# Kernel tuning notes

Measured on AMD Instinct MI355X. Metric: run time of the kernel, lower is better.

## Reference

```python
import jax, jax.numpy as jnp
import numpy as np

N = 50000      # nodes
E = 800000     # edges (avg degree 16)
D_IN = 18      # 3 fields x 6 timesteps
H = 128        # hidden_dim
HEADS = 4
DH = H // HEADS
D_OUT = 3
NEG = 0.2      # LeakyReLU slope
BN_EPS = 1e-5


def leaky(x):
    return jnp.where(x >= 0, x, NEG * x)


def segment_softmax(e, row, n):
    # numerically stable softmax over edges grouped by target node (axis 0)
    m = jax.ops.segment_max(e, row, num_segments=n)
    ex = jnp.exp(e - m[row])
    s = jax.ops.segment_sum(ex, row, num_segments=n)
    return ex / (s[row] + 1e-16)


def single_head_attn(x, row, col, Wv, b, a_src, a_dst):
    h = x @ Wv + b                                   # [N,H] values
    s_src = x @ a_src                                # [N] query scalar (dim=1)
    s_dst = x @ a_dst                                # [N] key scalar
    e = leaky(s_src[row] + s_dst[col])               # [E]
    alpha = segment_softmax(e, row, N)               # [E]
    return jax.ops.segment_sum(alpha[:, None] * h[col], row, num_segments=N)


def multi_head_attn(x, row, col, Wv, b, a_src, a_dst):
    h = jnp.einsum('nd,hde->nhe', x, Wv) + b         # [N,4,32] per-head values
    s_src = x @ a_src.T                              # [N,4] per-head Q (dim=1)
    s_dst = x @ a_dst.T                              # [N,4] per-head K (dim=1)
    e = leaky(s_src[row] + s_dst[col])               # [E,4]
    alpha = segment_softmax(e, row, N)               # [E,4]
    out = jax.ops.segment_sum(alpha[:, :, None] * h[col], row, num_segments=N)
    return out.reshape(N, HEADS * DH)                # concat heads -> [N,128]


def batch_norm_eval(x, g, bt, m, v):
    return (x - m) * jax.lax.rsqrt(v + BN_EPS) * g + bt


def setup_inputs() -> dict:
    key = jax.random.key(0)
    ks = jax.random.split(key, 16)
    rn = lambda k, shp, s=0.05: jax.random.normal(k, shp, dtype=jnp.float32) * s
    return {
        'x': rn(ks[0], (N, D_IN), 1.0),
        'edge_index': jax.random.randint(ks[1], (2, E), 0, N, dtype=jnp.int32),
        'W_in': rn(ks[2], (D_IN, H)),
        'b_in': jnp.zeros((H,), jnp.float32),
        'W_agg': rn(ks[3], (D_IN, H)),
        'b_agg': jnp.zeros((H,), jnp.float32),
        'sh_Wv': rn(ks[4], (2, H, H)),
        'sh_b': jnp.zeros((2, H), jnp.float32),
        'sh_asrc': rn(ks[5], (2, H)),
        'sh_adst': rn(ks[6], (2, H)),
        'mh_Wv': rn(ks[7], (HEADS, H, DH)),
        'mh_b': jnp.zeros((HEADS, DH), jnp.float32),
        'mh_asrc': rn(ks[8], (HEADS, H)),
        'mh_adst': rn(ks[9], (HEADS, H)),
        'bn_gamma': jnp.ones((3, H), jnp.float32),
        'bn_beta': jnp.zeros((3, H), jnp.float32),
        'bn_mean': jnp.zeros((3, H), jnp.float32),
        'bn_var': jnp.ones((3, H), jnp.float32),
        'W_o1': rn(ks[10], (H, H)),
        'b_o1': jnp.zeros((H,), jnp.float32),
        'W_o2': rn(ks[11], (H, D_OUT), 0.01),
        'b_o2': jnp.zeros((D_OUT,), jnp.float32),
    }


def reference(x, edge_index, W_in, b_in, W_agg, b_agg, sh_Wv, sh_b, sh_asrc, sh_adst,
              mh_Wv, mh_b, mh_asrc, mh_adst, bn_gamma, bn_beta, bn_mean, bn_var,
              W_o1, b_o1, W_o2, b_o2):
    row, col = edge_index[0], edge_index[1]

    # explicit neighbor mean aggregation (fused gather-scatter)
    nsum = jax.ops.segment_sum(x[col], row, num_segments=N)     # [N,D_IN]
    deg = jax.ops.segment_sum(jnp.ones((E,), x.dtype), row, num_segments=N)
    nmean = nsum / (deg[:, None] + 1e-8)

    h = (x @ W_in + b_in) + (nmean @ W_agg + b_agg)             # [N,H]
    x0 = h

    # layer 0: single-head attention + BN + residual(x0) + leaky
    h1 = single_head_attn(h, row, col, sh_Wv[0], sh_b[0], sh_asrc[0], sh_adst[0])
    h1 = batch_norm_eval(h1, bn_gamma[0], bn_beta[0], bn_mean[0], bn_var[0])
    h = leaky(x0 + h1)

    # layer 1: multi-head (4 heads, Q/K dim=1) + BN, no residual (i=1), leaky
    h2 = multi_head_attn(h, row, col, mh_Wv, mh_b, mh_asrc, mh_adst)
    h2 = batch_norm_eval(h2, bn_gamma[1], bn_beta[1], bn_mean[1], bn_var[1])
    h = leaky(h2)

    # layer 2: single-head + BN + residual + leaky
    r = h
    h3 = single_head_attn(h, row, col, sh_Wv[1], sh_b[1], sh_asrc[1], sh_adst[1])
    h3 = batch_norm_eval(h3, bn_gamma[2], bn_beta[2], bn_mean[2], bn_var[2])
    h = leaky(r + h3)

    # output head (dropout is a no-op in eval)
    delta = leaky(h @ W_o1 + b_o1) @ W_o2 + b_o2                # [N,3]

    # residual skip from last timestep of the input sequence
    return x[:, -D_OUT:] + delta
```

## Files before the change

### kernel.cpp

```cpp
#include <hip/hip_runtime.h>
#include <math.h>

#define DIN 18
#define HID 128
#define NEGS 0.2f
#define BN_EPS 1e-5f
#define SCHUNK 2048

typedef unsigned short ushort_t;
typedef __attribute__((ext_vector_type(8))) short bf16x8;
typedef __attribute__((ext_vector_type(4))) float f32x4;

__device__ __forceinline__ float leaky(float x){ return x >= 0.f ? x : NEGS * x; }

__device__ __forceinline__ float wred_sum(float v){
  #pragma unroll
  for (int off = 32; off; off >>= 1) v += __shfl_xor(v, off);
  return v;
}

__device__ __forceinline__ ushort_t f2bf(float f){
  union { float f; unsigned u; } v; v.f = f;
  unsigned r = v.u + 0x7FFFu + ((v.u >> 16) & 1u);
  return (ushort_t)(r >> 16);
}
__device__ __forceinline__ float bf_lo(unsigned p){ return __uint_as_float(p << 16); }
__device__ __forceinline__ float bf_hi(unsigned p){ return __uint_as_float(p & 0xFFFF0000u); }

__device__ __forceinline__ float sel4(float v0, float v1, float v2, float v3, int hd){
  float a = (hd & 1) ? v1 : v0;
  float b = (hd & 1) ? v3 : v2;
  return (hd & 2) ? b : a;
}

__global__ void k_deg(const int* __restrict__ row, int* __restrict__ deg, int E){
  int i = blockIdx.x * blockDim.x + threadIdx.x;
  if (i < E) atomicAdd(&deg[row[i]], 1);
}

__global__ void k_scan1(const int* __restrict__ deg, int* __restrict__ bsum, int n){
  __shared__ int wtot[4];
  int tid = threadIdx.x, lane = tid & 63, wid = tid >> 6;
  int base = blockIdx.x * SCHUNK + tid * 8;
  int acc = 0;
  #pragma unroll
  for (int j = 0; j < 8; ++j){
    int i = base + j;
    if (i < n) acc += deg[i];
  }
  #pragma unroll
  for (int off = 32; off; off >>= 1) acc += __shfl_xor(acc, off);
  if (lane == 0) wtot[wid] = acc;
  __syncthreads();
  if (tid == 0) bsum[blockIdx.x] = wtot[0] + wtot[1] + wtot[2] + wtot[3];
}

__global__ void k_scan2(int* __restrict__ bsum, int nb){
  int lane = threadIdx.x;
  int carry = 0;
  for (int base = 0; base < nb; base += 64){
    int i = base + lane;
    int v = (i < nb) ? bsum[i] : 0;
    #pragma unroll
    for (int off = 1; off < 64; off <<= 1){
      int u = __shfl_up(v, off);
      if (lane >= off) v += u;
    }
    if (i < nb) bsum[i] = v + carry;
    carry += __shfl(v, 63);
  }
}

__global__ void k_scan3(const int* __restrict__ deg, const int* __restrict__ bsum,
                        int* __restrict__ rowptr, int n){
  __shared__ int wtot[4];
  int tid = threadIdx.x, lane = tid & 63, wid = tid >> 6;
  int base = blockIdx.x * SCHUNK + tid * 8;
  int l[8];
  int acc = 0;
  #pragma unroll
  for (int j = 0; j < 8; ++j){
    int i = base + j;
    acc += (i < n) ? deg[i] : 0;
    l[j] = acc;
  }
  int v = acc;
  #pragma unroll
  for (int off = 1; off < 64; off <<= 1){
    int u = __shfl_up(v, off);
    if (lane >= off) v += u;
  }
  if (lane == 63) wtot[wid] = v;
  __syncthreads();
  int woff = 0;
  for (int w = 0; w < wid; ++w) woff += wtot[w];
  int boff = (blockIdx.x == 0) ? 0 : bsum[blockIdx.x - 1];
  int tpre = boff + woff + (v - acc);
  #pragma unroll
  for (int j = 0; j < 8; ++j){
    int i = base + j;
    if (i < n) rowptr[i + 1] = tpre + l[j];
  }
  if (blockIdx.x == 0 && tid == 0) rowptr[0] = 0;
}

__global__ void k_fill(const int* __restrict__ row, const int* __restrict__ col,
                       const int* __restrict__ rowptr, int* __restrict__ cursor,
                       int* __restrict__ cols_s, int E){
  int i = blockIdx.x * blockDim.x + threadIdx.x;
  if (i < E){
    int r = row[i];
    int p = atomicAdd(&cursor[r], 1);
    cols_s[rowptr[r] + p] = col[i];
  }
}

__global__ void k_nmean(const float* __restrict__ x, const int* __restrict__ rowptr,
                        const int* __restrict__ cols, float* __restrict__ nmean, int n){
  __shared__ int s_cv[4][64];
  int wid = threadIdx.x >> 6;
  int node = blockIdx.x * 4 + wid;
  if (node >= n) return;
  int lane = threadIdx.x & 63;
  int s = rowptr[node], e = rowptr[node + 1];
  float acc = 0.f;
  for (int j0 = s; j0 < e; j0 += 64){
    int len = min(64, e - j0);
    int cv = (lane < len) ? cols[j0 + lane] : 0;
    s_cv[wid][lane] = cv;
    int k = 0;
    for (; k + 4 <= len; k += 4){
      int c0 = s_cv[wid][k], c1 = s_cv[wid][k+1], c2 = s_cv[wid][k+2], c3 = s_cv[wid][k+3];
      if (lane < DIN){
        float v0 = x[c0 * DIN + lane], v1 = x[c1 * DIN + lane];
        float v2 = x[c2 * DIN + lane], v3 = x[c3 * DIN + lane];
        acc += (v0 + v1) + (v2 + v3);
      }
    }
    for (; k < len; ++k){
      int c = s_cv[wid][k];
      if (lane < DIN) acc += x[c * DIN + lane];
    }
  }
  if (lane < DIN){
    float d = (float)(e - s);
    nmean[node * DIN + lane] = acc / (d + 1e-8f);
  }
}

__global__ void k_h_in(const float* __restrict__ x, const float* __restrict__ nmean,
                       const float* __restrict__ Win, const float* __restrict__ bin,
                       const float* __restrict__ Wagg, const float* __restrict__ bagg,
                       float* __restrict__ out, int n){
  int wid = threadIdx.x >> 6;
  int node = blockIdx.x * 4 + wid;
  if (node >= n) return;
  int lane = threadIdx.x & 63;
  float xv = 0.f;
  if (lane < DIN) xv = x[node * DIN + lane];
  else if (lane < 2 * DIN) xv = nmean[node * DIN + (lane - DIN)];
  float acc0 = bin[lane]      + bagg[lane];
  float acc1 = bin[64 + lane] + bagg[64 + lane];
  #pragma unroll
  for (int d = 0; d < DIN; ++d){
    float xd = __shfl(xv, d);
    float nd = __shfl(xv, DIN + d);
    acc0 += xd * Win[d * HID + lane]       + nd * Wagg[d * HID + lane];
    acc1 += xd * Win[d * HID + 64 + lane]  + nd * Wagg[d * HID + 64 + lane];
  }
  out[node * HID + lane]      = acc0;
  out[node * HID + 64 + lane] = acc1;
}

__global__ void k_wt_sh(const float* __restrict__ W, ushort_t* __restrict__ Wt){
  int i = blockIdx.x * 256 + threadIdx.x;
  int c = i >> 7, d = i & 127;
  Wt[c * HID + d] = f2bf(W[d * HID + c]);
}
__global__ void k_wt_mh(const float* __restrict__ mhWv, ushort_t* __restrict__ Wt){
  int i = blockIdx.x * 256 + threadIdx.x;
  int c = i >> 7, d = i & 127;
  Wt[c * HID + d] = f2bf(mhWv[((c >> 5) * HID + d) * 32 + (c & 31)]);
}

__global__ void k_gemm_mfma(const float* __restrict__ A, const ushort_t* __restrict__ Bt,
                            const float* __restrict__ bias, ushort_t* __restrict__ dstb,
                            float* __restrict__ dstf, int n, int mode){
  int wv = threadIdx.x >> 6, lane = threadIdx.x & 63;
  int r0 = blockIdx.x * 64 + wv * 16;
  int lr = lane & 15, lk = lane >> 4;
  int arow = r0 + lr; if (arow >= n) arow = n - 1;
  const float* Ap = A + (size_t)arow * HID + lk * 8;
  bf16x8 a[4];
  #pragma unroll
  for (int kb = 0; kb < 4; ++kb){
    float4 lo = *(const float4*)(Ap + kb * 32);
    float4 hi = *(const float4*)(Ap + kb * 32 + 4);
    bf16x8 t;
    t[0] = (short)f2bf(lo.x); t[1] = (short)f2bf(lo.y);
    t[2] = (short)f2bf(lo.z); t[3] = (short)f2bf(lo.w);
    t[4] = (short)f2bf(hi.x); t[5] = (short)f2bf(hi.y);
    t[6] = (short)f2bf(hi.z); t[7] = (short)f2bf(hi.w);
    a[kb] = t;
  }
  f32x4 acc[8];
  #pragma unroll
  for (int t = 0; t < 8; ++t) acc[t] = (f32x4){0.f, 0.f, 0.f, 0.f};
  #pragma unroll
  for (int t = 0; t < 8; ++t){
    const ushort_t* Bp = Bt + (size_t)(t * 16 + lr) * HID + lk * 8;
    #pragma unroll
    for (int kb = 0; kb < 4; ++kb){
      bf16x8 b = *(const bf16x8*)(Bp + kb * 32);
      acc[t] = __builtin_amdgcn_mfma_f32_16x16x32_bf16(a[kb], b, acc[t], 0, 0, 0);
    }
  }
  #pragma unroll
  for (int t = 0; t < 8; ++t){
    int col = t * 16 + lr;
    float bs = bias[col];
    #pragma unroll
    for (int j = 0; j < 4; ++j){
      int rr = r0 + lk * 4 + j;
      if (rr < n){
        float v = acc[t][j] + bs;
        if (mode == 2) dstb[(size_t)rr * HID + col] = f2bf(v);
        else           dstf[(size_t)rr * HID + col] = leaky(v);
      }
    }
  }
}

__global__ void k_scores_sh(const float* __restrict__ h, const float* __restrict__ asrc,
                            const float* __restrict__ adst,
                            float* __restrict__ ssrc, float* __restrict__ sdst, int n){
  int node = blockIdx.x * 4 + (threadIdx.x >> 6);
  if (node >= n) return;
  int lane = threadIdx.x & 63;
  float h0 = h[node * HID + lane], h1 = h[node * HID + 64 + lane];
  float ps = h0 * asrc[lane] + h1 * asrc[64 + lane];
  float pd = h0 * adst[lane] + h1 * adst[64 + lane];
  ps = wred_sum(ps);
  pd = wred_sum(pd);
  if (lane == 0){ ssrc[node] = ps; sdst[node] = pd; }
}

__global__ void k_scores_mh(const float* __restrict__ h, const float* __restrict__ asrc,
                            const float* __restrict__ adst,
                            float* __restrict__ ssrc, float* __restrict__ sdst, int n){
  int node = blockIdx.x * 4 + (threadIdx.x >> 6);
  if (node >= n) return;
  int lane = threadIdx.x & 63;
  float h0 = h[node * HID + lane], h1 = h[node * HID + 64 + lane];
  #pragma unroll
  for (int hd = 0; hd < 4; ++hd){
    float ps = h0 * asrc[hd * HID + lane] + h1 * asrc[hd * HID + 64 + lane];
    float pd = h0 * adst[hd * HID + lane] + h1 * adst[hd * HID + 64 + lane];
    ps = wred_sum(ps);
    pd = wred_sum(pd);
    if (lane == 0){ ssrc[node * 4 + hd] = ps; sdst[node * 4 + hd] = pd; }
  }
}

__global__ void k_agg_sh(const int* __restrict__ rowptr, const int* __restrict__ cols,
                         const float* __restrict__ ssrc, const float* __restrict__ sdst,
                         const ushort_t* __restrict__ hv, const float* __restrict__ resid,
                         const float* __restrict__ bng, const float* __restrict__ bnb,
                         const float* __restrict__ bnm, const float* __restrict__ bnv,
                         float* __restrict__ out, int n){
  __shared__ int   s_cv[4][64];
  __shared__ float s_ex[4][64];
  int wid = threadIdx.x >> 6;
  int node = blockIdx.x * 4 + wid;
  if (node >= n) return;
  int lane = threadIdx.x & 63;
  const unsigned* hv32 = (const unsigned*)hv;
  int s = rowptr[node], e = rowptr[node + 1];
  float sq = ssrc[node];
  float ssum = 0.f, a0 = 0.f, a1 = 0.f;
  for (int j0 = s; j0 < e; j0 += 64){
    int len = min(64, e - j0);
    int cv = 0; float ex = 0.f;
    if (lane < len){
      cv = cols[j0 + lane];
      ex = __expf(leaky(sq + sdst[cv]));
    }
    ssum += ex;
    s_cv[wid][lane] = cv;
    s_ex[wid][lane] = ex;
    int k = 0;
    for (; k + 4 <= len; k += 4){
      int c0 = s_cv[wid][k],   c1 = s_cv[wid][k+1];
      int c2 = s_cv[wid][k+2], c3 = s_cv[wid][k+3];
      float l0 = s_ex[wid][k],   l1 = s_ex[wid][k+1];
      float l2 = s_ex[wid][k+2], l3 = s_ex[wid][k+3];
      unsigned p0 = hv32[c0 * 64 + lane], p1 = hv32[c1 * 64 + lane];
      unsigned p2 = hv32[c2 * 64 + lane], p3 = hv32[c3 * 64 + lane];
      a0 += l0 * bf_lo(p0); a1 += l0 * bf_hi(p0);
      a0 += l1 * bf_lo(p1); a1 += l1 * bf_hi(p1);
      a0 += l2 * bf_lo(p2); a1 += l2 * bf_hi(p2);
      a0 += l3 * bf_lo(p3); a1 += l3 * bf_hi(p3);
    }
    for (; k < len; ++k){
      int c = s_cv[wid][k];
      float l = s_ex[wid][k];
      unsigned p = hv32[c * 64 + lane];
      a0 += l * bf_lo(p); a1 += l * bf_hi(p);
    }
  }
  ssum = wred_sum(ssum);
  float inv = 1.f / (ssum + 1e-16f);
  a0 *= inv; a1 *= inv;
  int d0 = 2 * lane, d1 = 2 * lane + 1;
  float v0 = (a0 - bnm[d0]) * rsqrtf(bnv[d0] + BN_EPS) * bng[d0] + bnb[d0];
  float v1 = (a1 - bnm[d1]) * rsqrtf(bnv[d1] + BN_EPS) * bng[d1] + bnb[d1];
  if (resid){ v0 += resid[node * HID + d0]; v1 += resid[node * HID + d1]; }
  out[node * HID + d0] = leaky(v0);
  out[node * HID + d1] = leaky(v1);
}

__global__ void k_agg_mh(const int* __restrict__ rowptr, const int* __restrict__ cols,
                         const float* __restrict__ ssrc, const float* __restrict__ sdst,
                         const ushort_t* __restrict__ hv,
                         const float* __restrict__ bng, const float* __restrict__ bnb,
                         const float* __restrict__ bnm, const float* __restrict__ bnv,
                         float* __restrict__ out, int n){
  __shared__ int    s_cv[4][64];
  __shared__ float4 s_ex[4][64];
  int wid = threadIdx.x >> 6;
  int node = blockIdx.x * 4 + wid;
  if (node >= n) return;
  int lane = threadIdx.x & 63;
  const unsigned* hv32 = (const unsigned*)hv;
  int s = rowptr[node], e = rowptr[node + 1];
  const float4 sq = *(const float4*)&ssrc[node * 4];
  int hd = lane >> 4;
  float s0 = 0.f, s1 = 0.f, s2 = 0.f, s3 = 0.f;
  float a0 = 0.f, a1 = 0.f;
  const float* exw = &s_ex[wid][0].x;
  for (int j0 = s; j0 < e; j0 += 64){
    int len = min(64, e - j0);
    int cv = 0;
    float e0 = 0.f, e1 = 0.f, e2 = 0.f, e3 = 0.f;
    if (lane < len){
      cv = cols[j0 + lane];
      float4 kd = *(const float4*)&sdst[cv * 4];
      e0 = __expf(leaky(sq.x + kd.x)); e1 = __expf(leaky(sq.y + kd.y));
      e2 = __expf(leaky(sq.z + kd.z)); e3 = __expf(leaky(sq.w + kd.w));
    }
    s0 += e0; s1 += e1; s2 += e2; s3 += e3;
    s_cv[wid][lane] = cv;
    s_ex[wid][lane] = make_float4(e0, e1, e2, e3);
    int k = 0;
    for (; k + 4 <= len; k += 4){
      int c0 = s_cv[wid][k],   c1 = s_cv[wid][k+1];
      int c2 = s_cv[wid][k+2], c3 = s_cv[wid][k+3];
      float l0 = exw[(k)   * 4 + hd], l1 = exw[(k+1) * 4 + hd];
      float l2 = exw[(k+2) * 4 + hd], l3 = exw[(k+3) * 4 + hd];
      unsigned p0 = hv32[c0 * 64 + lane], p1 = hv32[c1 * 64 + lane];
      unsigned p2 = hv32[c2 * 64 + lane], p3 = hv32[c3 * 64 + lane];
      a0 += l0 * bf_lo(p0); a1 += l0 * bf_hi(p0);
      a0 += l1 * bf_lo(p1); a1 += l1 * bf_hi(p1);
      a0 += l2 * bf_lo(p2); a1 += l2 * bf_hi(p2);
      a0 += l3 * bf_lo(p3); a1 += l3 * bf_hi(p3);
    }
    for (; k < len; ++k){
      int c = s_cv[wid][k];
      float l = exw[k * 4 + hd];
      unsigned p = hv32[c * 64 + lane];
      a0 += l * bf_lo(p); a1 += l * bf_hi(p);
    }
  }
  s0 = wred_sum(s0); s1 = wred_sum(s1);
  s2 = wred_sum(s2); s3 = wred_sum(s3);
  float i0 = 1.f / (s0 + 1e-16f), i1 = 1.f / (s1 + 1e-16f);
  float i2 = 1.f / (s2 + 1e-16f), i3 = 1.f / (s3 + 1e-16f);
  float ih = sel4(i0, i1, i2, i3, hd);
  a0 *= ih; a1 *= ih;
  int d0 = 2 * lane, d1 = 2 * lane + 1;
  float v0 = (a0 - bnm[d0]) * rsqrtf(bnv[d0] + BN_EPS) * bng[d0] + bnb[d0];
  float v1 = (a1 - bnm[d1]) * rsqrtf(bnv[d1] + BN_EPS) * bng[d1] + bnb[d1];
  out[node * HID + d0] = leaky(v0);
  out[node * HID + d1] = leaky(v1);
}

__global__ void k_out(const float* __restrict__ o1, const float* __restrict__ Wo2,
                      const float* __restrict__ bo2, const float* __restrict__ x,
                      float* __restrict__ out, int n){
  int node = blockIdx.x * 4 + (threadIdx.x >> 6);
  if (node >= n) return;
  int lane = threadIdx.x & 63;
  float a = o1[node * HID + lane], b = o1[node * HID + 64 + lane];
  float p0 = a * Wo2[lane * 3 + 0] + b * Wo2[(lane + 64) * 3 + 0];
  float p1 = a * Wo2[lane * 3 + 1] + b * Wo2[(lane + 64) * 3 + 1];
  float p2 = a * Wo2[lane * 3 + 2] + b * Wo2[(lane + 64) * 3 + 2];
  p0 = wred_sum(p0); p1 = wred_sum(p1); p2 = wred_sum(p2);
  if (lane == 0){
    out[node * 3 + 0] = x[node * DIN + 15] + p0 + bo2[0];
    out[node * 3 + 1] = x[node * DIN + 16] + p1 + bo2[1];
    out[node * 3 + 2] = x[node * DIN + 17] + p2 + bo2[2];
  }
}

extern "C" void kernel_launch(void* const* d_in, const int* in_sizes, int n_in,
                              void* d_out, int out_size, void* d_ws, size_t ws_size,
                              hipStream_t stream){
  const float* x       = (const float*)d_in[0];
  const int*   ei      = (const int*)  d_in[1];
  const float* W_in    = (const float*)d_in[2];
  const float* b_in    = (const float*)d_in[3];
  const float* W_agg   = (const float*)d_in[4];
  const float* b_agg   = (const float*)d_in[5];
  const float* sh_Wv   = (const float*)d_in[6];
  const float* sh_b    = (const float*)d_in[7];
  const float* sh_asrc = (const float*)d_in[8];
  const float* sh_adst = (const float*)d_in[9];
  const float* mh_Wv   = (const float*)d_in[10];
  const float* mh_b    = (const float*)d_in[11];
  const float* mh_asrc = (const float*)d_in[12];
  const float* mh_adst = (const float*)d_in[13];
  const float* bn_g    = (const float*)d_in[14];
  const float* bn_bt   = (const float*)d_in[15];
  const float* bn_m    = (const float*)d_in[16];
  const float* bn_v    = (const float*)d_in[17];
  const float* W_o1    = (const float*)d_in[18];
  const float* b_o1    = (const float*)d_in[19];
  const float* W_o2    = (const float*)d_in[20];
  const float* b_o2    = (const float*)d_in[21];
  float* out = (float*)d_out;

  const int N = in_sizes[0] / DIN;
  const int E = in_sizes[1] / 2;
  const int* row = ei;
  const int* col = ei + E;

  char* w = (char*)d_ws;
  size_t off = 0;
  auto alloc = [&](size_t bytes) -> void* {
    void* p = w + off;
    off = (off + bytes + 255) & ~(size_t)255;
    return p;
  };
  int*      tmp    = (int*)     alloc((size_t)N * 4);
  int*      rowptr = (int*)     alloc((size_t)(N + 1) * 4);
  int*      cols_s = (int*)     alloc((size_t)E * 4);
  int*      bsum   = (int*)     alloc((size_t)1024 * 4);
  float*    nmean  = (float*)   alloc((size_t)N * DIN * 4);
  float*    ssrc   = (float*)   alloc((size_t)N * 4 * 4);
  float*    sdst   = (float*)   alloc((size_t)N * 4 * 4);
  ushort_t* wt0    = (ushort_t*)alloc((size_t)HID * HID * 2);
  ushort_t* wt1    = (ushort_t*)alloc((size_t)HID * HID * 2);
  ushort_t* wt2    = (ushort_t*)alloc((size_t)HID * HID * 2);
  ushort_t* wt3    = (ushort_t*)alloc((size_t)HID * HID * 2);
  float*    buf0   = (float*)   alloc((size_t)N * HID * 4);
  float*    buf1   = (float*)   alloc((size_t)N * HID * 4);
  float*    buf2   = (float*)   alloc((size_t)N * HID * 4);
  ushort_t* hvb    = (ushort_t*)alloc((size_t)N * HID * 2);

  const int eb = (E + 255) / 256;
  const int nb4 = (N + 3) / 4;
  const int gb = (N + 63) / 64;
  const int nsb = (N + SCHUNK - 1) / SCHUNK;

  hipMemsetAsync(tmp, 0, (size_t)N * 4, stream);
  k_deg<<<eb, 256, 0, stream>>>(row, tmp, E);
  k_scan1<<<nsb, 256, 0, stream>>>(tmp, bsum, N);
  k_scan2<<<1, 64, 0, stream>>>(bsum, nsb);
  k_scan3<<<nsb, 256, 0, stream>>>(tmp, bsum, rowptr, N);
  hipMemsetAsync(tmp, 0, (size_t)N * 4, stream);
  k_fill<<<eb, 256, 0, stream>>>(row, col, rowptr, tmp, cols_s, E);

  k_wt_sh<<<64, 256, 0, stream>>>(sh_Wv, wt0);
  k_wt_mh<<<64, 256, 0, stream>>>(mh_Wv, wt1);
  k_wt_sh<<<64, 256, 0, stream>>>(sh_Wv + HID * HID, wt2);
  k_wt_sh<<<64, 256, 0, stream>>>(W_o1, wt3);

  k_nmean<<<nb4, 256, 0, stream>>>(x, rowptr, cols_s, nmean, N);
  k_h_in<<<nb4, 256, 0, stream>>>(x, nmean, W_in, b_in, W_agg, b_agg, buf0, N);

  k_gemm_mfma<<<gb, 256, 0, stream>>>(buf0, wt0, sh_b, hvb, nullptr, N, 2);
  k_scores_sh<<<nb4, 256, 0, stream>>>(buf0, sh_asrc, sh_adst, ssrc, sdst, N);
  k_agg_sh<<<nb4, 256, 0, stream>>>(rowptr, cols_s, ssrc, sdst, hvb, buf0,
                                    bn_g, bn_bt, bn_m, bn_v, buf1, N);

  k_gemm_mfma<<<gb, 256, 0, stream>>>(buf1, wt1, mh_b, hvb, nullptr, N, 2);
  k_scores_mh<<<nb4, 256, 0, stream>>>(buf1, mh_asrc, mh_adst, ssrc, sdst, N);
  k_agg_mh<<<nb4, 256, 0, stream>>>(rowptr, cols_s, ssrc, sdst, hvb,
                                    bn_g + HID, bn_bt + HID, bn_m + HID, bn_v + HID, buf0, N);

  k_gemm_mfma<<<gb, 256, 0, stream>>>(buf0, wt2, sh_b + HID, hvb, nullptr, N, 2);
  k_scores_sh<<<nb4, 256, 0, stream>>>(buf0, sh_asrc + HID, sh_adst + HID, ssrc, sdst, N);
  k_agg_sh<<<nb4, 256, 0, stream>>>(rowptr, cols_s, ssrc, sdst, hvb, buf0,
                                    bn_g + 2 * HID, bn_bt + 2 * HID, bn_m + 2 * HID, bn_v + 2 * HID,
                                    buf1, N);

  k_gemm_mfma<<<gb, 256, 0, stream>>>(buf1, wt3, b_o1, nullptr, buf2, N, 1);
  k_out<<<nb4, 256, 0, stream>>>(buf2, W_o2, b_o2, x, out, N);
}
```

Before: 434.6 us.

## Fuse attention score computation into producer epilogues and precompute CSR ranks

Attention score dot products are computed in the epilogue of the kernel that produces each layer's input (input projection and the aggregation kernels), removing separate score kernels that reread the full hidden activations. The CSR build stores each edge's atomic rank during degree counting so the fill becomes an atomic-free scatter. This adds a rank buffer and extra wave reductions inside aggregation kernels, possibly raising register pressure.

```diff
diff --git a/kernel.cpp b/kernel.cpp
--- a/kernel.cpp
+++ b/kernel.cpp
@@ -33,9 +33,10 @@
   return (hd & 2) ? b : a;
 }
 
-__global__ void k_deg(const int* __restrict__ row, int* __restrict__ deg, int E){
+__global__ void k_deg_rank(const int* __restrict__ row, int* __restrict__ deg,
+                           int* __restrict__ rank, int E){
   int i = blockIdx.x * blockDim.x + threadIdx.x;
-  if (i < E) atomicAdd(&deg[row[i]], 1);
+  if (i < E) rank[i] = atomicAdd(&deg[row[i]], 1);
 }
 
 __global__ void k_scan1(const int* __restrict__ deg, int* __restrict__ bsum, int n){
@@ -104,14 +105,12 @@
   if (blockIdx.x == 0 && tid == 0) rowptr[0] = 0;
 }
 
-__global__ void k_fill(const int* __restrict__ row, const int* __restrict__ col,
-                       const int* __restrict__ rowptr, int* __restrict__ cursor,
-                       int* __restrict__ cols_s, int E){
+__global__ void k_scatter(const int* __restrict__ row, const int* __restrict__ col,
+                          const int* __restrict__ rowptr, const int* __restrict__ rank,
+                          int* __restrict__ cols_s, int E){
   int i = blockIdx.x * blockDim.x + threadIdx.x;
   if (i < E){
-    int r = row[i];
-    int p = atomicAdd(&cursor[r], 1);
-    cols_s[rowptr[r] + p] = col[i];
+    cols_s[rowptr[row[i]] + rank[i]] = col[i];
   }
 }
 
@@ -151,6 +150,8 @@
 __global__ void k_h_in(const float* __restrict__ x, const float* __restrict__ nmean,
                        const float* __restrict__ Win, const float* __restrict__ bin,
                        const float* __restrict__ Wagg, const float* __restrict__ bagg,
+                       const float* __restrict__ asrc, const float* __restrict__ adst,
+                       float* __restrict__ ssrc, float* __restrict__ sdst,
                        float* __restrict__ out, int n){
   int wid = threadIdx.x >> 6;
   int node = blockIdx.x * 4 + wid;
@@ -170,6 +171,11 @@
   }
   out[node * HID + lane]      = acc0;
   out[node * HID + 64 + lane] = acc1;
+  float ps = acc0 * asrc[lane] + acc1 * asrc[64 + lane];
+  float pd = acc0 * adst[lane] + acc1 * adst[64 + lane];
+  ps = wred_sum(ps);
+  pd = wred_sum(pd);
+  if (lane == 0){ ssrc[node] = ps; sdst[node] = pd; }
 }
 
 __global__ void k_wt_sh(const float* __restrict__ W, ushort_t* __restrict__ Wt){
@@ -231,42 +237,13 @@
   }
 }
 
-__global__ void k_scores_sh(const float* __restrict__ h, const float* __restrict__ asrc,
-                            const float* __restrict__ adst,
-                            float* __restrict__ ssrc, float* __restrict__ sdst, int n){
-  int node = blockIdx.x * 4 + (threadIdx.x >> 6);
-  if (node >= n) return;
-  int lane = threadIdx.x & 63;
-  float h0 = h[node * HID + lane], h1 = h[node * HID + 64 + lane];
-  float ps = h0 * asrc[lane] + h1 * asrc[64 + lane];
-  float pd = h0 * adst[lane] + h1 * adst[64 + lane];
-  ps = wred_sum(ps);
-  pd = wred_sum(pd);
-  if (lane == 0){ ssrc[node] = ps; sdst[node] = pd; }
-}
-
-__global__ void k_scores_mh(const float* __restrict__ h, const float* __restrict__ asrc,
-                            const float* __restrict__ adst,
-                            float* __restrict__ ssrc, float* __restrict__ sdst, int n){
-  int node = blockIdx.x * 4 + (threadIdx.x >> 6);
-  if (node >= n) return;
-  int lane = threadIdx.x & 63;
-  float h0 = h[node * HID + lane], h1 = h[node * HID + 64 + lane];
-  #pragma unroll
-  for (int hd = 0; hd < 4; ++hd){
-    float ps = h0 * asrc[hd * HID + lane] + h1 * asrc[hd * HID + 64 + lane];
-    float pd = h0 * adst[hd * HID + lane] + h1 * adst[hd * HID + 64 + lane];
-    ps = wred_sum(ps);
-    pd = wred_sum(pd);
-    if (lane == 0){ ssrc[node * 4 + hd] = ps; sdst[node * 4 + hd] = pd; }
-  }
-}
-
 __global__ void k_agg_sh(const int* __restrict__ rowptr, const int* __restrict__ cols,
                          const float* __restrict__ ssrc, const float* __restrict__ sdst,
                          const ushort_t* __restrict__ hv, const float* __restrict__ resid,
                          const float* __restrict__ bng, const float* __restrict__ bnb,
                          const float* __restrict__ bnm, const float* __restrict__ bnv,
+                         const float* __restrict__ masrc, const float* __restrict__ madst,
+                         float* __restrict__ ossrc, float* __restrict__ osdst,
                          float* __restrict__ out, int n){
   __shared__ int   s_cv[4][64];
   __shared__ float s_ex[4][64];
@@ -315,8 +292,19 @@
   float v0 = (a0 - bnm[d0]) * rsqrtf(bnv[d0] + BN_EPS) * bng[d0] + bnb[d0];
   float v1 = (a1 - bnm[d1]) * rsqrtf(bnv[d1] + BN_EPS) * bng[d1] + bnb[d1];
   if (resid){ v0 += resid[node * HID + d0]; v1 += resid[node * HID + d1]; }
-  out[node * HID + d0] = leaky(v0);
-  out[node * HID + d1] = leaky(v1);
+  float o0 = leaky(v0), o1 = leaky(v1);
+  out[node * HID + d0] = o0;
+  out[node * HID + d1] = o1;
+  if (ossrc){
+    #pragma unroll
+    for (int h = 0; h < 4; ++h){
+      float ps = o0 * masrc[h * HID + d0] + o1 * masrc[h * HID + d1];
+      float pd = o0 * madst[h * HID + d0] + o1 * madst[h * HID + d1];
+      ps = wred_sum(ps);
+      pd = wred_sum(pd);
+      if (lane == 0){ ossrc[node * 4 + h] = ps; osdst[node * 4 + h] = pd; }
+    }
+  }
 }
 
 __global__ void k_agg_mh(const int* __restrict__ rowptr, const int* __restrict__ cols,
@@ -324,6 +312,8 @@
                          const ushort_t* __restrict__ hv,
                          const float* __restrict__ bng, const float* __restrict__ bnb,
                          const float* __restrict__ bnm, const float* __restrict__ bnv,
+                         const float* __restrict__ sasrc, const float* __restrict__ sadst,
+                         float* __restrict__ ossrc, float* __restrict__ osdst,
                          float* __restrict__ out, int n){
   __shared__ int    s_cv[4][64];
   __shared__ float4 s_ex[4][64];
@@ -380,8 +370,14 @@
   int d0 = 2 * lane, d1 = 2 * lane + 1;
   float v0 = (a0 - bnm[d0]) * rsqrtf(bnv[d0] + BN_EPS) * bng[d0] + bnb[d0];
   float v1 = (a1 - bnm[d1]) * rsqrtf(bnv[d1] + BN_EPS) * bng[d1] + bnb[d1];
-  out[node * HID + d0] = leaky(v0);
-  out[node * HID + d1] = leaky(v1);
+  float o0 = leaky(v0), o1 = leaky(v1);
+  out[node * HID + d0] = o0;
+  out[node * HID + d1] = o1;
+  float ps = o0 * sasrc[d0] + o1 * sasrc[d1];
+  float pd = o0 * sadst[d0] + o1 * sadst[d1];
+  ps = wred_sum(ps);
+  pd = wred_sum(pd);
+  if (lane == 0){ ossrc[node] = ps; osdst[node] = pd; }
 }
 
 __global__ void k_out(const float* __restrict__ o1, const float* __restrict__ Wo2,
@@ -444,10 +440,13 @@
   int*      tmp    = (int*)     alloc((size_t)N * 4);
   int*      rowptr = (int*)     alloc((size_t)(N + 1) * 4);
   int*      cols_s = (int*)     alloc((size_t)E * 4);
+  int*      rank   = (int*)     alloc((size_t)E * 4);
   int*      bsum   = (int*)     alloc((size_t)1024 * 4);
   float*    nmean  = (float*)   alloc((size_t)N * DIN * 4);
-  float*    ssrc   = (float*)   alloc((size_t)N * 4 * 4);
-  float*    sdst   = (float*)   alloc((size_t)N * 4 * 4);
+  float*    ssrcA  = (float*)   alloc((size_t)N * 4);
+  float*    sdstA  = (float*)   alloc((size_t)N * 4);
+  float*    ssrcB  = (float*)   alloc((size_t)N * 4 * 4);
+  float*    sdstB  = (float*)   alloc((size_t)N * 4 * 4);
   ushort_t* wt0    = (ushort_t*)alloc((size_t)HID * HID * 2);
   ushort_t* wt1    = (ushort_t*)alloc((size_t)HID * HID * 2);
   ushort_t* wt2    = (ushort_t*)alloc((size_t)HID * HID * 2);
@@ -463,12 +462,11 @@
   const int nsb = (N + SCHUNK - 1) / SCHUNK;
 
   hipMemsetAsync(tmp, 0, (size_t)N * 4, stream);
-  k_deg<<<eb, 256, 0, stream>>>(row, tmp, E);
+  k_deg_rank<<<eb, 256, 0, stream>>>(row, tmp, rank, E);
   k_scan1<<<nsb, 256, 0, stream>>>(tmp, bsum, N);
   k_scan2<<<1, 64, 0, stream>>>(bsum, nsb);
   k_scan3<<<nsb, 256, 0, stream>>>(tmp, bsum, rowptr, N);
-  hipMemsetAsync(tmp, 0, (size_t)N * 4, stream);
-  k_fill<<<eb, 256, 0, stream>>>(row, col, rowptr, tmp, cols_s, E);
+  k_scatter<<<eb, 256, 0, stream>>>(row, col, rowptr, rank, cols_s, E);
 
   k_wt_sh<<<64, 256, 0, stream>>>(sh_Wv, wt0);
   k_wt_mh<<<64, 256, 0, stream>>>(mh_Wv, wt1);
@@ -476,23 +474,23 @@
   k_wt_sh<<<64, 256, 0, stream>>>(W_o1, wt3);
 
   k_nmean<<<nb4, 256, 0, stream>>>(x, rowptr, cols_s, nmean, N);
-  k_h_in<<<nb4, 256, 0, stream>>>(x, nmean, W_in, b_in, W_agg, b_agg, buf0, N);
+  k_h_in<<<nb4, 256, 0, stream>>>(x, nmean, W_in, b_in, W_agg, b_agg,
+                                  sh_asrc, sh_adst, ssrcA, sdstA, buf0, N);
 
   k_gemm_mfma<<<gb, 256, 0, stream>>>(buf0, wt0, sh_b, hvb, nullptr, N, 2);
-  k_scores_sh<<<nb4, 256, 0, stream>>>(buf0, sh_asrc, sh_adst, ssrc, sdst, N);
-  k_agg_sh<<<nb4, 256, 0, stream>>>(rowptr, cols_s, ssrc, sdst, hvb, buf0,
-                                    bn_g, bn_bt, bn_m, bn_v, buf1, N);
+  k_agg_sh<<<nb4, 256, 0, stream>>>(rowptr, cols_s, ssrcA, sdstA, hvb, buf0,
+                                    bn_g, bn_bt, bn_m, bn_v,
+                                    mh_asrc, mh_adst, ssrcB, sdstB, buf1, N);
 
   k_gemm_mfma<<<gb, 256, 0, stream>>>(buf1, wt1, mh_b, hvb, nullptr, N, 2);
-  k_scores_mh<<<nb4, 256, 0, stream>>>(buf1, mh_asrc, mh_adst, ssrc, sdst, N);
-  k_agg_mh<<<nb4, 256, 0, stream>>>(rowptr, cols_s, ssrc, sdst, hvb,
-                                    bn_g + HID, bn_bt + HID, bn_m + HID, bn_v + HID, buf0, N);
+  k_agg_mh<<<nb4, 256, 0, stream>>>(rowptr, cols_s, ssrcB, sdstB, hvb,
+                                    bn_g + HID, bn_bt + HID, bn_m + HID, bn_v + HID,
+                                    sh_asrc + HID, sh_adst + HID, ssrcA, sdstA, buf0, N);
 
   k_gemm_mfma<<<gb, 256, 0, stream>>>(buf0, wt2, sh_b + HID, hvb, nullptr, N, 2);
-  k_scores_sh<<<nb4, 256, 0, stream>>>(buf0, sh_asrc + HID, sh_adst + HID, ssrc, sdst, N);
-  k_agg_sh<<<nb4, 256, 0, stream>>>(rowptr, cols_s, ssrc, sdst, hvb, buf0,
+  k_agg_sh<<<nb4, 256, 0, stream>>>(rowptr, cols_s, ssrcA, sdstA, hvb, buf0,
                                     bn_g + 2 * HID, bn_bt + 2 * HID, bn_m + 2 * HID, bn_v + 2 * HID,
-                                    buf1, N);
+                                    nullptr, nullptr, nullptr, nullptr, buf1, N);
 
   k_gemm_mfma<<<gb, 256, 0, stream>>>(buf1, wt3, b_o1, nullptr, buf2, N, 1);
   k_out<<<nb4, 256, 0, stream>>>(buf2, W_o2, b_o2, x, out, N);
```

Result: faster. 380.9 us (-12.4%).
